# Kernel optimization log

Measured on AMD Instinct MI355X. Metric: run time of the kernel, lower is better.

The kernel has to match this reference:

```python
import jax, jax.numpy as jnp
import numpy as np

N, D = 16384, 32            # nodes, max neighbors (0-padded)
INP, U = 256, 128           # input_units, units
R, ENT = 8, 8               # relations, entity types (relation/entity id 0 = padding for relations)


def setup_inputs() -> dict:
    key = jax.random.key(0)
    ks = jax.random.split(key, 12)
    s = 0.05  # scale learned params for numerical sanity (torch init is raw randn)
    return {
        "node_state": jax.random.normal(ks[0], (N, INP), dtype=jnp.float32),
        "adjacency": jax.random.randint(ks[1], (N, D), 0, N + 1, dtype=jnp.int32),  # 0 = pad row
        "point_enc": jax.random.randint(ks[2], (N,), 0, ENT, dtype=jnp.int32),
        "relation_enc": jax.random.randint(ks[3], (N, D), 0, R, dtype=jnp.int32),   # 0 = pad edge
        "point_enc_w": jax.random.normal(ks[4], (ENT, INP, U), dtype=jnp.float32) * s,
        "relation_enc_w": jax.random.normal(ks[5], (R, U, U), dtype=jnp.float32) * s,
        "q_w": jax.random.normal(ks[6], (U, U), dtype=jnp.float32) * s,
        "k_w": jax.random.normal(ks[7], (U, U), dtype=jnp.float32) * s,
        "v_w": jax.random.normal(ks[8], (U, U), dtype=jnp.float32) * s,
        "fc_w": jax.random.normal(ks[9], (U, U), dtype=jnp.float32) * s,
        "fc_b": jax.random.normal(ks[10], (U,), dtype=jnp.float32) * s,
    }


def reference(node_state, adjacency, point_enc, relation_enc,
              point_enc_w, relation_enc_w, q_w, k_w, v_w, fc_w, fc_b):
    ent, inp, u = point_enc_w.shape
    r_cnt = relation_enc_w.shape[0]
    dt = node_state.dtype

    # center = node_state @ point_enc_w[point_enc]; loop over small fixed entity set
    # to avoid materializing an (N, INP, U) gathered weight tensor.
    center = jnp.zeros((node_state.shape[0], u), dtype=dt)
    for e in range(ent):
        center = center + jnp.where(point_enc[:, None] == e,
                                    node_state @ point_enc_w[e], 0.0)

    # prepend zero row: adjacency index 0 == padding neighbor
    padded = jnp.concatenate([jnp.zeros((1, u), dtype=dt), center], axis=0)  # (N+1, U)
    x = padded[adjacency]  # (N, D, U) gathered neighbor embeddings

    # neighbors = x @ relation_enc_w[relation_enc]; per-relation GEMM + mask
    # (same math as the per-edge gathered matmul, without the E*U*U blowup)
    neighbors = jnp.zeros_like(x)
    for r in range(r_cnt):
        neighbors = neighbors + jnp.where(relation_enc[..., None] == r,
                                          jnp.einsum('ndu,uv->ndv', x, relation_enc_w[r]), 0.0)

    scale = u ** 0.5
    q = (center @ q_w) / scale                               # (N, U)
    k = jnp.einsum('ndu,uv->ndv', neighbors, k_w) / scale    # (N, D, U)
    v = jnp.einsum('ndu,uv->ndv', neighbors, v_w)            # (N, D, U)

    scores = jnp.einsum('nu,ndu->nd', q, k)                  # (N, D)
    scores = jnp.where(relation_enc == 0, jnp.asarray(-1e9, dt), scores)
    attn = jax.nn.softmax(scores, axis=-1)                   # over neighbors
    agg = jnp.einsum('nd,ndu->nu', attn, v)                  # (N, U)

    return center + jax.nn.relu(agg @ fc_w + fc_b)           # (N, U)
```

## Files before the change

### kernel.cpp

```cpp
#include <hip/hip_runtime.h>

#define NNODE 16384
#define DD 32
#define INPC 256
#define UC 128
#define RC 8
#define EC 8

typedef __attribute__((ext_vector_type(8))) short short8;
typedef __attribute__((ext_vector_type(4))) float float4v;
typedef __attribute__((ext_vector_type(4))) unsigned uint4v;

__device__ __forceinline__ unsigned short f2bf(float f) {
    unsigned u = __builtin_bit_cast(unsigned, f);
    unsigned r = (u + 0x7FFFu + ((u >> 16) & 1u)) >> 16;
    return (unsigned short)r;
}
__device__ __forceinline__ float bf2f(unsigned short s) { return __builtin_bit_cast(float, (unsigned)s << 16); }

template <int CTRL>
__device__ __forceinline__ float dppq(float x) {
    return __builtin_bit_cast(float,
        __builtin_amdgcn_mov_dpp(__builtin_bit_cast(int, x), CTRL, 0xF, 0xF, true));
}
#define DPP_XOR1 0xB1
#define DPP_XOR2 0x4E

__device__ __forceinline__ short8 ld8bf(const float* p) {
    float4 v0 = *(const float4*)p;
    float4 v1 = *(const float4*)(p + 4);
    short8 a;
    a[0] = (short)f2bf(v0.x); a[1] = (short)f2bf(v0.y);
    a[2] = (short)f2bf(v0.z); a[3] = (short)f2bf(v0.w);
    a[4] = (short)f2bf(v1.x); a[5] = (short)f2bf(v1.y);
    a[6] = (short)f2bf(v1.z); a[7] = (short)f2bf(v1.w);
    return a;
}

__device__ __forceinline__ int bfrag_idx(int k, int col, int nct) {
    int ks = k >> 5, ct = col >> 4;
    int l = (((k >> 3) & 3) << 4) | (col & 15);
    return (((ks * nct + ct) << 6) + l) * 8 + (k & 7);
}

__global__ void k_setup(const float* __restrict__ pew, const float* __restrict__ qw,
                        const float* __restrict__ kw, const float* __restrict__ relw,
                        const float* __restrict__ vw, const float* __restrict__ fcw,
                        const int* __restrict__ pe,
                        unsigned short* __restrict__ pewfrag,
                        unsigned short* __restrict__ BallQfrag, unsigned short* __restrict__ RVFfrag,
                        int* __restrict__ blockhist) {
    __shared__ unsigned short stage_s[128 * 132];
    __shared__ unsigned short mat_s[16 * 136];
    __shared__ int hh[8];
    int b = blockIdx.x;
    if (b < 1024) {
        int id = b * 256 + threadIdx.x;
        int e = id >> 15, k = (id >> 7) & 255, col = id & 127;
        pewfrag[(e << 15) + bfrag_idx(k, col, 8)] = f2bf(pew[id]);
        return;
    }
    if (b < 1088) {
        int pb = b - 1024;
        int r = pb & 7, i0 = (pb >> 3) * 16;
        int w = threadIdx.x >> 6, l = threadIdx.x & 63;
        int mrow = l & 15, kgrp = (l >> 4) << 3;
        const float* R = relw + r * (UC * UC);

        float4v accP[2] = {};
        #pragma unroll
        for (int ks = 0; ks < 4; ++ks) {
            short8 a = ld8bf(&qw[(i0 + mrow) * UC + ks * 32 + kgrp]);
            #pragma unroll
            for (int ci = 0; ci < 2; ++ci) {
                int ct = w * 2 + ci;
                short8 bf = ld8bf(&kw[(ct * 16 + mrow) * UC + ks * 32 + kgrp]);
                accP[ci] = __builtin_amdgcn_mfma_f32_16x16x32_bf16(a, bf, accP[ci], 0, 0, 0);
            }
        }
        #pragma unroll
        for (int ci = 0; ci < 2; ++ci)
            #pragma unroll
            for (int reg = 0; reg < 4; ++reg) {
                int row = ((l >> 4) << 2) + reg;
                int col = (w * 2 + ci) * 16 + mrow;
                mat_s[row * 136 + col] = f2bf(accP[ci][reg] * (1.0f / 128.0f));
            }
        for (int it = 0; it < 16; ++it) {
            int idx = it * 256 + threadIdx.x;
            int row = idx >> 5, col = (idx & 31) * 4;
            float4 v = *(const float4*)&vw[row * UC + col];
            uint2 o;
            o.x = (unsigned)f2bf(v.x) | ((unsigned)f2bf(v.y) << 16);
            o.y = (unsigned)f2bf(v.z) | ((unsigned)f2bf(v.w) << 16);
            *(uint2*)&stage_s[row * 132 + col] = o;
        }
        __syncthreads();

        float4v accM[2] = {}, accV[2] = {};
        #pragma unroll
        for (int ks = 0; ks < 4; ++ks) {
            short8 aM = *(const short8*)&mat_s[mrow * 136 + ks * 32 + kgrp];
            short8 aV = ld8bf(&R[(i0 + mrow) * UC + ks * 32 + kgrp]);
            #pragma unroll
            for (int ci = 0; ci < 2; ++ci) {
                int ct = w * 2 + ci;
                short8 bM = ld8bf(&R[(ct * 16 + mrow) * UC + ks * 32 + kgrp]);
                accM[ci] = __builtin_amdgcn_mfma_f32_16x16x32_bf16(aM, bM, accM[ci], 0, 0, 0);
                uint4v pv;
                #pragma unroll
                for (int jp = 0; jp < 4; ++jp) {
                    unsigned e0 = stage_s[(ks * 32 + kgrp + jp * 2) * 132 + ct * 16 + mrow];
                    unsigned e1 = stage_s[(ks * 32 + kgrp + jp * 2 + 1) * 132 + ct * 16 + mrow];
                    pv[jp] = e0 | (e1 << 16);
                }
                accV[ci] = __builtin_amdgcn_mfma_f32_16x16x32_bf16(
                    aV, __builtin_bit_cast(short8, pv), accV[ci], 0, 0, 0);
            }
        }
        #pragma unroll
        for (int ci = 0; ci < 2; ++ci)
            #pragma unroll
            for (int reg = 0; reg < 4; ++reg) {
                int i = i0 + ((l >> 4) << 2) + reg;
                int col = r * 128 + (w * 2 + ci) * 16 + mrow;
                BallQfrag[bfrag_idx(i, col, 64)] = f2bf(accM[ci][reg]);
            }
        __syncthreads();
        #pragma unroll
        for (int ci = 0; ci < 2; ++ci)
            #pragma unroll
            for (int reg = 0; reg < 4; ++reg)
                mat_s[(((l >> 4) << 2) + reg) * 136 + (w * 2 + ci) * 16 + mrow] = f2bf(accV[ci][reg]);
        for (int it = 0; it < 16; ++it) {
            int idx = it * 256 + threadIdx.x;
            int row = idx >> 5, col = (idx & 31) * 4;
            float4 v = *(const float4*)&fcw[row * UC + col];
            uint2 o;
            o.x = (unsigned)f2bf(v.x) | ((unsigned)f2bf(v.y) << 16);
            o.y = (unsigned)f2bf(v.z) | ((unsigned)f2bf(v.w) << 16);
            *(uint2*)&stage_s[row * 132 + col] = o;
        }
        __syncthreads();

        float4v accF[2] = {};
        #pragma unroll
        for (int ks = 0; ks < 4; ++ks) {
            short8 aF = *(const short8*)&mat_s[mrow * 136 + ks * 32 + kgrp];
            #pragma unroll
            for (int ci = 0; ci < 2; ++ci) {
                int ct = w * 2 + ci;
                uint4v pv;
                #pragma unroll
                for (int jp = 0; jp < 4; ++jp) {
                    unsigned e0 = stage_s[(ks * 32 + kgrp + jp * 2) * 132 + ct * 16 + mrow];
                    unsigned e1 = stage_s[(ks * 32 + kgrp + jp * 2 + 1) * 132 + ct * 16 + mrow];
                    pv[jp] = e0 | (e1 << 16);
                }
                accF[ci] = __builtin_amdgcn_mfma_f32_16x16x32_bf16(
                    aF, __builtin_bit_cast(short8, pv), accF[ci], 0, 0, 0);
            }
        }
        #pragma unroll
        for (int ci = 0; ci < 2; ++ci)
            #pragma unroll
            for (int reg = 0; reg < 4; ++reg) {
                int i = i0 + ((l >> 4) << 2) + reg;
                int col = (w * 2 + ci) * 16 + mrow;
                RVFfrag[bfrag_idx(r * 128 + i, col, 8)] = f2bf(accF[ci][reg]);
            }
        return;
    }
    {
        int hb = b - 1088;
        if (threadIdx.x < 8) hh[threadIdx.x] = 0;
        __syncthreads();
        atomicAdd(&hh[pe[hb * 256 + threadIdx.x]], 1);
        __syncthreads();
        if (threadIdx.x < 8) blockhist[hb * 8 + threadIdx.x] = hh[threadIdx.x];
    }
}

__global__ void k_scatter(const int* __restrict__ pe, const int* __restrict__ blockhist,
                          int* __restrict__ list, int* __restrict__ cnt, int* __restrict__ basep) {
    __shared__ int boff[8];
    __shared__ int totS[8], exS[8];
    __shared__ int wavecnt[4 * 8];
    int t = threadIdx.x, w = t >> 6, l = t & 63;
    if (w == 0) {
        #pragma unroll
        for (int e = 0; e < 8; ++e) {
            int h = blockhist[l * 8 + e];
            int pref = h;
            #pragma unroll
            for (int off = 1; off < 64; off <<= 1) {
                int v = __shfl_up(pref, off, 64);
                pref += (l >= off) ? v : 0;
            }
            if (l == (int)blockIdx.x) exS[e] = pref - h;
            if (l == 63) totS[e] = pref;
        }
    }
    __syncthreads();
    if (t == 0) {
        int run = 0;
        #pragma unroll
        for (int e = 0; e < 8; ++e) {
            boff[e] = run + exS[e];
            if (blockIdx.x == 0) { basep[e] = run; cnt[e] = totS[e]; }
            run += totS[e];
        }
    }
    __syncthreads();
    int n = blockIdx.x * 256 + t;
    int e = pe[n];
    unsigned long long mymask = 0;
    #pragma unroll
    for (int r = 0; r < 8; ++r) {
        unsigned long long m = __ballot(e == r);
        if (e == r) mymask = m;
        if (l == r) wavecnt[w * 8 + r] = (int)__popcll(m);
    }
    __syncthreads();
    int off = 0;
    for (int w2 = 0; w2 < w; ++w2) off += wavecnt[w2 * 8 + e];
    unsigned long long ltmask = (1ull << l) - 1ull;
    int rank = (int)__popcll(mymask & ltmask);
    list[boff[e] + off + rank] = n;
}

__global__ __launch_bounds__(256, 4)
void k_center(const float* __restrict__ ns, const unsigned short* __restrict__ pewfrag,
              const int* __restrict__ list, const int* __restrict__ cnt,
              const int* __restrict__ base, unsigned short* __restrict__ center_bf) {
    int e = blockIdx.y;
    int c = cnt[e];
    int start = blockIdx.x * 16;
    if (start >= c) return;
    int w = threadIdx.x >> 6, l = threadIdx.x & 63;

    int rid = list[base[e] + min(start + (l & 15), c - 1)];

    float4v acc[2] = {};
    const unsigned short* pf = pewfrag + ((size_t)e << 15);
    #pragma unroll
    for (int ks = 0; ks < 8; ++ks) {
        short8 a = ld8bf(&ns[(size_t)rid * 256 + ks * 32 + ((l >> 4) << 3)]);
        #pragma unroll
        for (int ci = 0; ci < 2; ++ci) {
            int ct = w * 2 + ci;
            short8 b = *(const short8*)&pf[(((ks * 8 + ct) << 6) + l) * 8];
            acc[ci] = __builtin_amdgcn_mfma_f32_16x16x32_bf16(a, b, acc[ci], 0, 0, 0);
        }
    }
    #pragma unroll
    for (int reg = 0; reg < 4; ++reg) {
        int row16 = start + ((l >> 4) << 2) + reg;
        if (row16 < c) {
            int gid = list[base[e] + row16];
            #pragma unroll
            for (int ci = 0; ci < 2; ++ci)
                center_bf[(size_t)gid * 128 + (w * 2 + ci) * 16 + (l & 15)] = f2bf(acc[ci][reg]);
        }
    }
}

#define QSTRIDE 1096
__global__ __launch_bounds__(256, 2)
void k_final(const unsigned short* __restrict__ center_bf,
             const unsigned short* __restrict__ BallQfrag,
             const unsigned short* __restrict__ RVFfrag,
             const int* __restrict__ adj, const int* __restrict__ rel,
             const float* __restrict__ fcb, float* __restrict__ out) {
    __shared__ unsigned short qlds[16 * QSTRIDE];
    __shared__ __align__(16) unsigned short xs[4][4096];
    int w = threadIdx.x >> 6, l = threadIdx.x & 63;
    int n0 = blockIdx.x * 16;

    int aiq[4][2], rvq[4][2], rvrow[4][2];
    #pragma unroll
    for (int q = 0; q < 4; ++q) {
        int n = n0 + w * 4 + q;
        #pragma unroll
        for (int t = 0; t < 2; ++t) {
            aiq[q][t] = adj[n * DD + t * 16 + (l & 15)];
            rvq[q][t] = rel[n * DD + t * 16 + (l & 15)];
            rvrow[q][t] = aiq[q][t] > 0 ? aiq[q][t] - 1 : 0;
        }
    }

    short8 xp[2][4];
    #pragma unroll
    for (int t = 0; t < 2; ++t)
        #pragma unroll
        for (int ks = 0; ks < 4; ++ks)
            xp[t][ks] = *(const short8*)&center_bf[(size_t)rvrow[0][t] * 128 + ks * 32 + ((l >> 4) << 3)];

    {
        short8 a[4];
        #pragma unroll
        for (int ks = 0; ks < 4; ++ks)
            a[ks] = *(const short8*)&center_bf[(size_t)(n0 + (l & 15)) * 128 + ks * 32 + ((l >> 4) << 3)];
        for (int ci = 0; ci < 16; ++ci) {
            int ct = w * 16 + ci;
            float4v acc = {};
            #pragma unroll
            for (int ks = 0; ks < 4; ++ks) {
                short8 b = *(const short8*)&BallQfrag[(((ks * 64 + ct) << 6) + l) * 8];
                acc = __builtin_amdgcn_mfma_f32_16x16x32_bf16(a[ks], b, acc, 0, 0, 0);
            }
            int r = ct >> 3;
            int ch = (ct & 7) * 16 + (l & 15);
            #pragma unroll
            for (int reg = 0; reg < 4; ++reg) {
                int rn = ((l >> 4) << 2) + reg;
                qlds[rn * QSTRIDE + r * 136 + ch] = f2bf(acc[reg]);
            }
        }
    }
    __syncthreads();

    unsigned short* xsw = &xs[w][0];

    #pragma unroll
    for (int q = 0; q < 4; ++q) {
        int tn = w * 4 + q;
        int ai0 = aiq[q][0], ai1 = aiq[q][1];
        int rv0 = rvq[q][0], rv1 = rvq[q][1];

        {
            int G = l >> 4;
            #pragma unroll
            for (int t = 0; t < 2; ++t) {
                int edge = t * 16 + (l & 15);
                int est = edge >> 2;
                int slot = (edge & 3) ^ (est & 3);
                int base = est * 64 + slot * 16 + (G & 1) * 8;
                #pragma unroll
                for (int ks = 0; ks < 4; ++ks)
                    *(short8*)&xsw[(ks * 2 + (G >> 1)) * 512 + base] = xp[t][ks];
            }
        }

        float4v sc[2] = {};
        #pragma unroll
        for (int ks = 0; ks < 4; ++ks) {
            short8 qb = *(const short8*)&qlds[tn * QSTRIDE + (l & 7) * 136 + ks * 32 + ((l >> 4) << 3)];
            sc[0] = __builtin_amdgcn_mfma_f32_16x16x32_bf16(qb, xp[0][ks], sc[0], 0, 0, 0);
            sc[1] = __builtin_amdgcn_mfma_f32_16x16x32_bf16(qb, xp[1][ks], sc[1], 0, 0, 0);
        }

        if (q < 3) {
            #pragma unroll
            for (int t = 0; t < 2; ++t)
                #pragma unroll
                for (int ks = 0; ks < 4; ++ks)
                    xp[t][ks] = *(const short8*)&center_bf[(size_t)rvrow[q + 1][t] * 128
                                                           + ks * 32 + ((l >> 4) << 3)];
        }

        float sel0, sel1;
        {
            int r = rv0;
            float v01 = (r & 1) ? sc[0][1] : sc[0][0];
            float v23 = (r & 1) ? sc[0][3] : sc[0][2];
            float regv = (r & 2) ? v23 : v01;
            float s = __shfl(regv, ((r >> 2) << 4) | (l & 15), 64);
            if (ai0 == 0) s = 0.f;
            if (r == 0) s = -1e9f;
            sel0 = fminf(s, 60.f);
        }
        {
            int r = rv1;
            float v01 = (r & 1) ? sc[1][1] : sc[1][0];
            float v23 = (r & 1) ? sc[1][3] : sc[1][2];
            float regv = (r & 2) ? v23 : v01;
            float s = __shfl(regv, ((r >> 2) << 4) | (l & 15), 64);
            if (ai1 == 0) s = 0.f;
            if (r == 0) s = -1e9f;
            sel1 = fminf(s, 60.f);
        }

        float at0 = __expf(sel0);
        float at1 = __expf(sel1);
        float sm = at0 + at1;
        sm += dppq<DPP_XOR1>(sm);
        sm += dppq<DPP_XOR2>(sm);
        sm += __shfl_xor(sm, 4, 64);
        sm += __shfl_xor(sm, 8, 64);
        float inv = 1.0f / fmaxf(sm, 1e-30f);
        at0 *= inv; at1 *= inv;
        if (ai0 == 0) at0 = 0.f;
        if (ai1 == 0) at1 = 0.f;

        unsigned md0 = (unsigned)f2bf(at0) | ((unsigned)rv0 << 16);
        unsigned md1 = (unsigned)f2bf(at1) | ((unsigned)rv1 << 16);
        unsigned mdsel = (l >= 32) ? md1 : md0;
        unsigned aw[4];
        #pragma unroll
        for (int jp = 0; jp < 4; ++jp) {
            unsigned m0 = __shfl(mdsel, (l & 48) | (((l >> 4) & 1) * 8 + jp * 2), 64);
            unsigned m1 = __shfl(mdsel, (l & 48) | (((l >> 4) & 1) * 8 + jp * 2 + 1), 64);
            unsigned s0 = ((m0 >> 16) == (unsigned)(l & 15)) ? (m0 & 0xFFFFu) : 0u;
            unsigned s1 = ((m1 >> 16) == (unsigned)(l & 15)) ? (m1 & 0xFFFFu) : 0u;
            aw[jp] = s0 | (s1 << 16);
        }
        uint4v av = {aw[0], aw[1], aw[2], aw[3]};
        short8 afrag = __builtin_bit_cast(short8, av);

        #pragma unroll
        for (int ct = 0; ct < 8; ++ct) {
            unsigned short p[8];
            #pragma unroll
            for (int jj = 0; jj < 8; ++jj) {
                int st = (l >> 4) * 2 + (jj >> 2);
                int slot = (jj & 3) ^ (st & 3);
                p[jj] = xsw[ct * 512 + st * 64 + slot * 16 + (l & 15)];
            }
            uint4v bv = {(unsigned)p[0] | ((unsigned)p[1] << 16),
                         (unsigned)p[2] | ((unsigned)p[3] << 16),
                         (unsigned)p[4] | ((unsigned)p[5] << 16),
                         (unsigned)p[6] | ((unsigned)p[7] << 16)};
            float4v zc = {};
            float4v acc = __builtin_amdgcn_mfma_f32_16x16x32_bf16(
                afrag, __builtin_bit_cast(short8, bv), zc, 0, 0, 0);
            if (l < 32) {
                int rbase = (l >> 4) << 2;
                #pragma unroll
                for (int reg = 0; reg < 4; ++reg)
                    qlds[tn * QSTRIDE + (rbase + reg) * 136 + ct * 16 + (l & 15)] = f2bf(acc[reg]);
            }
        }
    }
    __syncthreads();

    {
        float4v acc[2] = {};
        #pragma unroll 4
        for (int ks = 0; ks < 32; ++ks) {
            short8 a = *(const short8*)&qlds[(l & 15) * QSTRIDE + (ks >> 2) * 136
                                             + (ks & 3) * 32 + ((l >> 4) << 3)];
            #pragma unroll
            for (int ci = 0; ci < 2; ++ci) {
                int ct = w * 2 + ci;
                short8 b = *(const short8*)&RVFfrag[(((ks * 8 + ct) << 6) + l) * 8];
                acc[ci] = __builtin_amdgcn_mfma_f32_16x16x32_bf16(a, b, acc[ci], 0, 0, 0);
            }
        }
        #pragma unroll
        for (int ci = 0; ci < 2; ++ci) {
            int ct = w * 2 + ci;
            int col = ct * 16 + (l & 15);
            float bb = fcb[col];
            #pragma unroll
            for (int reg = 0; reg < 4; ++reg) {
                int n = n0 + ((l >> 4) << 2) + reg;
                float v = acc[ci][reg] + bb;
                v = v > 0.f ? v : 0.f;
                out[(size_t)n * 128 + col] = bf2f(center_bf[(size_t)n * 128 + col]) + v;
            }
        }
    }
}

extern "C" void kernel_launch(void* const* d_in, const int* in_sizes, int n_in,
                              void* d_out, int out_size, void* d_ws, size_t ws_size,
                              hipStream_t stream) {
    const float* node_state = (const float*)d_in[0];
    const int*   adjacency  = (const int*)d_in[1];
    const int*   point_enc  = (const int*)d_in[2];
    const int*   relation   = (const int*)d_in[3];
    const float* pew        = (const float*)d_in[4];
    const float* relw       = (const float*)d_in[5];
    const float* qw         = (const float*)d_in[6];
    const float* kw         = (const float*)d_in[7];
    const float* vw         = (const float*)d_in[8];
    const float* fcw        = (const float*)d_in[9];
    const float* fcb        = (const float*)d_in[10];
    float* out = (float*)d_out;

    char* ws = (char*)d_ws;
    unsigned short* BallQfrag = (unsigned short*)ws;  ws += 128 * 1024 * 2;
    unsigned short* RVFfrag   = (unsigned short*)ws;  ws += 1024 * 128 * 2;
    unsigned short* center_bf = (unsigned short*)ws;  ws += (size_t)NNODE * 128 * 2;
    unsigned short* pewfrag   = (unsigned short*)ws;  ws += 8 * 32768 * 2;
    int* blockhist            = (int*)ws;             ws += 64 * 8 * 4;
    int* cnt                  = (int*)ws;             ws += 32;
    int* basep                = (int*)ws;             ws += 32;
    int* list                 = (int*)ws;             ws += NNODE * 4;

    k_setup<<<1152, 256, 0, stream>>>(pew, qw, kw, relw, vw, fcw, point_enc,
                                      pewfrag, BallQfrag, RVFfrag, blockhist);
    k_scatter<<<64, 256, 0, stream>>>(point_enc, blockhist, list, cnt, basep);
    k_center<<<dim3(192, 8), 256, 0, stream>>>(node_state, pewfrag, list, cnt, basep, center_bf);
    k_final<<<NNODE / 16, 256, 0, stream>>>(center_bf, BallQfrag, RVFfrag,
                                            adjacency, relation, fcb, out);
}
```

Measured before the change: 160.6 us.

## Halve per-wave LDS staging by processing neighbor halves sequentially, raise occupancy

The per-wave LDS staging buffer for gathered neighbor rows is halved by storing only 16 edges at a time. The relation-bucketed attention aggregation now runs as two accumulating MFMA passes, one per neighbor half, instead of one. The smaller shared-memory footprint allows launch bounds to request 3 blocks per CU instead of 2. The trade-off is extra MFMAs and shuffles, a second LDS write phase, and register pressure from keeping 8 accumulators plus a copy of the second half live under the tighter bound.

```diff
diff --git a/kernel.cpp b/kernel.cpp
--- a/kernel.cpp
+++ b/kernel.cpp
@@ -266,14 +266,14 @@
 }
 
 #define QSTRIDE 1096
-__global__ __launch_bounds__(256, 2)
+__global__ __launch_bounds__(256, 3)
 void k_final(const unsigned short* __restrict__ center_bf,
              const unsigned short* __restrict__ BallQfrag,
              const unsigned short* __restrict__ RVFfrag,
              const int* __restrict__ adj, const int* __restrict__ rel,
              const float* __restrict__ fcb, float* __restrict__ out) {
     __shared__ unsigned short qlds[16 * QSTRIDE];
-    __shared__ __align__(16) unsigned short xs[4][4096];
+    __shared__ __align__(16) unsigned short xs[4][2048];
     int w = threadIdx.x >> 6, l = threadIdx.x & 63;
     int n0 = blockIdx.x * 16;
 
@@ -321,6 +321,14 @@
     __syncthreads();
 
     unsigned short* xsw = &xs[w][0];
+    int ebase = ((l >> 4) & 1) * 8;
+    int wbase;
+    {
+        int e = l & 15;
+        int est = e >> 2;
+        int slot = (e & 3) ^ est;
+        wbase = est * 64 + slot * 16 + ebase;
+    }
 
     #pragma unroll
     for (int q = 0; q < 4; ++q) {
@@ -328,20 +336,6 @@
         int ai0 = aiq[q][0], ai1 = aiq[q][1];
         int rv0 = rvq[q][0], rv1 = rvq[q][1];
 
-        {
-            int G = l >> 4;
-            #pragma unroll
-            for (int t = 0; t < 2; ++t) {
-                int edge = t * 16 + (l & 15);
-                int est = edge >> 2;
-                int slot = (edge & 3) ^ (est & 3);
-                int base = est * 64 + slot * 16 + (G & 1) * 8;
-                #pragma unroll
-                for (int ks = 0; ks < 4; ++ks)
-                    *(short8*)&xsw[(ks * 2 + (G >> 1)) * 512 + base] = xp[t][ks];
-            }
-        }
-
         float4v sc[2] = {};
         #pragma unroll
         for (int ks = 0; ks < 4; ++ks) {
@@ -349,6 +343,13 @@
             sc[0] = __builtin_amdgcn_mfma_f32_16x16x32_bf16(qb, xp[0][ks], sc[0], 0, 0, 0);
             sc[1] = __builtin_amdgcn_mfma_f32_16x16x32_bf16(qb, xp[1][ks], sc[1], 0, 0, 0);
         }
+
+        #pragma unroll
+        for (int ks = 0; ks < 4; ++ks)
+            *(short8*)&xsw[(ks * 2 + (l >> 5)) * 256 + wbase] = xp[0][ks];
+        short8 xh1[4];
+        #pragma unroll
+        for (int ks = 0; ks < 4; ++ks) xh1[ks] = xp[1][ks];
 
         if (q < 3) {
             #pragma unroll
@@ -395,41 +396,82 @@
 
         unsigned md0 = (unsigned)f2bf(at0) | ((unsigned)rv0 << 16);
         unsigned md1 = (unsigned)f2bf(at1) | ((unsigned)rv1 << 16);
-        unsigned mdsel = (l >= 32) ? md1 : md0;
-        unsigned aw[4];
-        #pragma unroll
-        for (int jp = 0; jp < 4; ++jp) {
-            unsigned m0 = __shfl(mdsel, (l & 48) | (((l >> 4) & 1) * 8 + jp * 2), 64);
-            unsigned m1 = __shfl(mdsel, (l & 48) | (((l >> 4) & 1) * 8 + jp * 2 + 1), 64);
-            unsigned s0 = ((m0 >> 16) == (unsigned)(l & 15)) ? (m0 & 0xFFFFu) : 0u;
-            unsigned s1 = ((m1 >> 16) == (unsigned)(l & 15)) ? (m1 & 0xFFFFu) : 0u;
-            aw[jp] = s0 | (s1 << 16);
-        }
-        uint4v av = {aw[0], aw[1], aw[2], aw[3]};
-        short8 afrag = __builtin_bit_cast(short8, av);
-
-        #pragma unroll
-        for (int ct = 0; ct < 8; ++ct) {
-            unsigned short p[8];
-            #pragma unroll
-            for (int jj = 0; jj < 8; ++jj) {
-                int st = (l >> 4) * 2 + (jj >> 2);
-                int slot = (jj & 3) ^ (st & 3);
-                p[jj] = xsw[ct * 512 + st * 64 + slot * 16 + (l & 15)];
-            }
-            uint4v bv = {(unsigned)p[0] | ((unsigned)p[1] << 16),
-                         (unsigned)p[2] | ((unsigned)p[3] << 16),
-                         (unsigned)p[4] | ((unsigned)p[5] << 16),
-                         (unsigned)p[6] | ((unsigned)p[7] << 16)};
-            float4v zc = {};
-            float4v acc = __builtin_amdgcn_mfma_f32_16x16x32_bf16(
-                afrag, __builtin_bit_cast(short8, bv), zc, 0, 0, 0);
-            if (l < 32) {
-                int rbase = (l >> 4) << 2;
+
+        float4v bacc[8] = {};
+
+        {
+            unsigned aw[4];
+            #pragma unroll
+            for (int jp = 0; jp < 4; ++jp) {
+                unsigned m0 = __shfl(md0, (l & 48) | (ebase + jp * 2), 64);
+                unsigned m1 = __shfl(md0, (l & 48) | (ebase + jp * 2 + 1), 64);
+                unsigned s0 = ((m0 >> 16) == (unsigned)(l & 15)) ? (m0 & 0xFFFFu) : 0u;
+                unsigned s1 = ((m1 >> 16) == (unsigned)(l & 15)) ? (m1 & 0xFFFFu) : 0u;
+                aw[jp] = (l < 32) ? (s0 | (s1 << 16)) : 0u;
+            }
+            uint4v av = {aw[0], aw[1], aw[2], aw[3]};
+            short8 afrag = __builtin_bit_cast(short8, av);
+            #pragma unroll
+            for (int ct = 0; ct < 8; ++ct) {
+                unsigned short p[8];
+                #pragma unroll
+                for (int jj = 0; jj < 8; ++jj) {
+                    int ep = ebase + jj;
+                    int st = ep >> 2;
+                    int slot = (ep & 3) ^ st;
+                    p[jj] = xsw[ct * 256 + st * 64 + slot * 16 + (l & 15)];
+                }
+                uint4v bv = {(unsigned)p[0] | ((unsigned)p[1] << 16),
+                             (unsigned)p[2] | ((unsigned)p[3] << 16),
+                             (unsigned)p[4] | ((unsigned)p[5] << 16),
+                             (unsigned)p[6] | ((unsigned)p[7] << 16)};
+                bacc[ct] = __builtin_amdgcn_mfma_f32_16x16x32_bf16(
+                    afrag, __builtin_bit_cast(short8, bv), bacc[ct], 0, 0, 0);
+            }
+        }
+
+        #pragma unroll
+        for (int ks = 0; ks < 4; ++ks)
+            *(short8*)&xsw[(ks * 2 + (l >> 5)) * 256 + wbase] = xh1[ks];
+
+        {
+            unsigned aw[4];
+            #pragma unroll
+            for (int jp = 0; jp < 4; ++jp) {
+                unsigned m0 = __shfl(md1, (l & 48) | (ebase + jp * 2), 64);
+                unsigned m1 = __shfl(md1, (l & 48) | (ebase + jp * 2 + 1), 64);
+                unsigned s0 = ((m0 >> 16) == (unsigned)(l & 15)) ? (m0 & 0xFFFFu) : 0u;
+                unsigned s1 = ((m1 >> 16) == (unsigned)(l & 15)) ? (m1 & 0xFFFFu) : 0u;
+                aw[jp] = (l < 32) ? (s0 | (s1 << 16)) : 0u;
+            }
+            uint4v av = {aw[0], aw[1], aw[2], aw[3]};
+            short8 afrag = __builtin_bit_cast(short8, av);
+            #pragma unroll
+            for (int ct = 0; ct < 8; ++ct) {
+                unsigned short p[8];
+                #pragma unroll
+                for (int jj = 0; jj < 8; ++jj) {
+                    int ep = ebase + jj;
+                    int st = ep >> 2;
+                    int slot = (ep & 3) ^ st;
+                    p[jj] = xsw[ct * 256 + st * 64 + slot * 16 + (l & 15)];
+                }
+                uint4v bv = {(unsigned)p[0] | ((unsigned)p[1] << 16),
+                             (unsigned)p[2] | ((unsigned)p[3] << 16),
+                             (unsigned)p[4] | ((unsigned)p[5] << 16),
+                             (unsigned)p[6] | ((unsigned)p[7] << 16)};
+                bacc[ct] = __builtin_amdgcn_mfma_f32_16x16x32_bf16(
+                    afrag, __builtin_bit_cast(short8, bv), bacc[ct], 0, 0, 0);
+            }
+        }
+
+        if (l < 32) {
+            int rbase = (l >> 4) << 2;
+            #pragma unroll
+            for (int ct = 0; ct < 8; ++ct)
                 #pragma unroll
                 for (int reg = 0; reg < 4; ++reg)
-                    qlds[tn * QSTRIDE + (rbase + reg) * 136 + ct * 16 + (l & 15)] = f2bf(acc[reg]);
-            }
+                    qlds[tn * QSTRIDE + (rbase + reg) * 136 + ct * 16 + (l & 15)] = f2bf(bacc[ct][reg]);
         }
     }
     __syncthreads();
```

Result: no change. 159.2 us (-0.9%).

## Gather neighbor rows from global memory instead of LDS transpose staging

Applied to the files above, without the earlier changes.

Removes the per-wave 32KB LDS staging buffer that transposed gathered neighbor embeddings for the aggregation MFMA. The B-fragments are now built by scalar 16-bit gathers straight from center_bf, with row indices broadcast by shuffle. Adjacency, relation and validity are packed into one int per edge, and launch bounds are raised to 4 blocks per CU, since the LDS cut allows higher occupancy. The cost is many more narrow global or L2 loads per wave and possible register pressure under the tighter launch bound.

```diff
diff --git a/kernel.cpp b/kernel.cpp
--- a/kernel.cpp
+++ b/kernel.cpp
@@ -266,26 +266,26 @@
 }
 
 #define QSTRIDE 1096
-__global__ __launch_bounds__(256, 2)
+__global__ __launch_bounds__(256, 4)
 void k_final(const unsigned short* __restrict__ center_bf,
              const unsigned short* __restrict__ BallQfrag,
              const unsigned short* __restrict__ RVFfrag,
              const int* __restrict__ adj, const int* __restrict__ rel,
              const float* __restrict__ fcb, float* __restrict__ out) {
     __shared__ unsigned short qlds[16 * QSTRIDE];
-    __shared__ __align__(16) unsigned short xs[4][4096];
     int w = threadIdx.x >> 6, l = threadIdx.x & 63;
     int n0 = blockIdx.x * 16;
 
-    int aiq[4][2], rvq[4][2], rvrow[4][2];
+    int pk[4][2];
     #pragma unroll
     for (int q = 0; q < 4; ++q) {
         int n = n0 + w * 4 + q;
         #pragma unroll
         for (int t = 0; t < 2; ++t) {
-            aiq[q][t] = adj[n * DD + t * 16 + (l & 15)];
-            rvq[q][t] = rel[n * DD + t * 16 + (l & 15)];
-            rvrow[q][t] = aiq[q][t] > 0 ? aiq[q][t] - 1 : 0;
+            int ai = adj[n * DD + t * 16 + (l & 15)];
+            int rv = rel[n * DD + t * 16 + (l & 15)];
+            int rr = ai > 0 ? ai - 1 : 0;
+            pk[q][t] = (rr << 5) | (rv << 1) | (ai != 0 ? 1 : 0);
         }
     }
 
@@ -294,7 +294,8 @@
     for (int t = 0; t < 2; ++t)
         #pragma unroll
         for (int ks = 0; ks < 4; ++ks)
-            xp[t][ks] = *(const short8*)&center_bf[(size_t)rvrow[0][t] * 128 + ks * 32 + ((l >> 4) << 3)];
+            xp[t][ks] = *(const short8*)&center_bf[(size_t)(pk[0][t] >> 5) * 128
+                                                   + ks * 32 + ((l >> 4) << 3)];
 
     {
         short8 a[4];
@@ -320,27 +321,12 @@
     }
     __syncthreads();
 
-    unsigned short* xsw = &xs[w][0];
-
     #pragma unroll
     for (int q = 0; q < 4; ++q) {
         int tn = w * 4 + q;
-        int ai0 = aiq[q][0], ai1 = aiq[q][1];
-        int rv0 = rvq[q][0], rv1 = rvq[q][1];
-
-        {
-            int G = l >> 4;
-            #pragma unroll
-            for (int t = 0; t < 2; ++t) {
-                int edge = t * 16 + (l & 15);
-                int est = edge >> 2;
-                int slot = (edge & 3) ^ (est & 3);
-                int base = est * 64 + slot * 16 + (G & 1) * 8;
-                #pragma unroll
-                for (int ks = 0; ks < 4; ++ks)
-                    *(short8*)&xsw[(ks * 2 + (G >> 1)) * 512 + base] = xp[t][ks];
-            }
-        }
+        int p0 = pk[q][0], p1 = pk[q][1];
+        int rv0 = (p0 >> 1) & 7, rv1 = (p1 >> 1) & 7;
+        int va0 = p0 & 1, va1 = p1 & 1;
 
         float4v sc[2] = {};
         #pragma unroll
@@ -350,12 +336,24 @@
             sc[1] = __builtin_amdgcn_mfma_f32_16x16x32_bf16(qb, xp[1][ks], sc[1], 0, 0, 0);
         }
 
+        int rsel = (l & 32) ? (p1 >> 5) : (p0 >> 5);
+        int rows[8];
+        #pragma unroll
+        for (int jj = 0; jj < 8; ++jj)
+            rows[jj] = __shfl(rsel, (l & 48) | (((l >> 4) & 1) * 8 + jj), 64);
+        unsigned short g0[4][8];
+        #pragma unroll
+        for (int ct = 0; ct < 4; ++ct)
+            #pragma unroll
+            for (int jj = 0; jj < 8; ++jj)
+                g0[ct][jj] = center_bf[(size_t)rows[jj] * 128 + ct * 16 + (l & 15)];
+
         if (q < 3) {
             #pragma unroll
             for (int t = 0; t < 2; ++t)
                 #pragma unroll
                 for (int ks = 0; ks < 4; ++ks)
-                    xp[t][ks] = *(const short8*)&center_bf[(size_t)rvrow[q + 1][t] * 128
+                    xp[t][ks] = *(const short8*)&center_bf[(size_t)(pk[q + 1][t] >> 5) * 128
                                                            + ks * 32 + ((l >> 4) << 3)];
         }
 
@@ -366,7 +364,7 @@
             float v23 = (r & 1) ? sc[0][3] : sc[0][2];
             float regv = (r & 2) ? v23 : v01;
             float s = __shfl(regv, ((r >> 2) << 4) | (l & 15), 64);
-            if (ai0 == 0) s = 0.f;
+            if (!va0) s = 0.f;
             if (r == 0) s = -1e9f;
             sel0 = fminf(s, 60.f);
         }
@@ -376,7 +374,7 @@
             float v23 = (r & 1) ? sc[1][3] : sc[1][2];
             float regv = (r & 2) ? v23 : v01;
             float s = __shfl(regv, ((r >> 2) << 4) | (l & 15), 64);
-            if (ai1 == 0) s = 0.f;
+            if (!va1) s = 0.f;
             if (r == 0) s = -1e9f;
             sel1 = fminf(s, 60.f);
         }
@@ -390,8 +388,8 @@
         sm += __shfl_xor(sm, 8, 64);
         float inv = 1.0f / fmaxf(sm, 1e-30f);
         at0 *= inv; at1 *= inv;
-        if (ai0 == 0) at0 = 0.f;
-        if (ai1 == 0) at1 = 0.f;
+        if (!va0) at0 = 0.f;
+        if (!va1) at1 = 0.f;
 
         unsigned md0 = (unsigned)f2bf(at0) | ((unsigned)rv0 << 16);
         unsigned md1 = (unsigned)f2bf(at1) | ((unsigned)rv1 << 16);
@@ -409,18 +407,35 @@
         short8 afrag = __builtin_bit_cast(short8, av);
 
         #pragma unroll
-        for (int ct = 0; ct < 8; ++ct) {
-            unsigned short p[8];
-            #pragma unroll
-            for (int jj = 0; jj < 8; ++jj) {
-                int st = (l >> 4) * 2 + (jj >> 2);
-                int slot = (jj & 3) ^ (st & 3);
-                p[jj] = xsw[ct * 512 + st * 64 + slot * 16 + (l & 15)];
-            }
-            uint4v bv = {(unsigned)p[0] | ((unsigned)p[1] << 16),
-                         (unsigned)p[2] | ((unsigned)p[3] << 16),
-                         (unsigned)p[4] | ((unsigned)p[5] << 16),
-                         (unsigned)p[6] | ((unsigned)p[7] << 16)};
+        for (int ct = 0; ct < 4; ++ct) {
+            uint4v bv = {(unsigned)g0[ct][0] | ((unsigned)g0[ct][1] << 16),
+                         (unsigned)g0[ct][2] | ((unsigned)g0[ct][3] << 16),
+                         (unsigned)g0[ct][4] | ((unsigned)g0[ct][5] << 16),
+                         (unsigned)g0[ct][6] | ((unsigned)g0[ct][7] << 16)};
+            float4v zc = {};
+            float4v acc = __builtin_amdgcn_mfma_f32_16x16x32_bf16(
+                afrag, __builtin_bit_cast(short8, bv), zc, 0, 0, 0);
+            if (l < 32) {
+                int rbase = (l >> 4) << 2;
+                #pragma unroll
+                for (int reg = 0; reg < 4; ++reg)
+                    qlds[tn * QSTRIDE + (rbase + reg) * 136 + ct * 16 + (l & 15)] = f2bf(acc[reg]);
+            }
+        }
+
+        unsigned short g1[4][8];
+        #pragma unroll
+        for (int c2 = 0; c2 < 4; ++c2)
+            #pragma unroll
+            for (int jj = 0; jj < 8; ++jj)
+                g1[c2][jj] = center_bf[(size_t)rows[jj] * 128 + (c2 + 4) * 16 + (l & 15)];
+        #pragma unroll
+        for (int c2 = 0; c2 < 4; ++c2) {
+            int ct = c2 + 4;
+            uint4v bv = {(unsigned)g1[c2][0] | ((unsigned)g1[c2][1] << 16),
+                         (unsigned)g1[c2][2] | ((unsigned)g1[c2][3] << 16),
+                         (unsigned)g1[c2][4] | ((unsigned)g1[c2][5] << 16),
+                         (unsigned)g1[c2][6] | ((unsigned)g1[c2][7] << 16)};
             float4v zc = {};
             float4v acc = __builtin_amdgcn_mfma_f32_16x16x32_bf16(
                 afrag, __builtin_bit_cast(short8, bv), zc, 0, 0, 0);
```

New measurement: 160.2 us. About the same (-0.3%).
